# Kernel optimization log

Measured on AMD Instinct MI355X. Metric: run time of the kernel, lower is better.

The kernel has to match this reference:

```python
import jax, jax.numpy as jnp
import numpy as np

NEG_INF = -1e30  # stands in for -math.inf in masked_fill; -inf itself also works in fp32


def setup_inputs() -> dict:
    key = jax.random.key(0)
    k1, k2, k3, k4, k5 = jax.random.split(key, 5)
    B, T, S, H = 32, 512, 1024, 1024
    query = jax.random.normal(k1, (B, T, H), dtype=jnp.float32)
    encoder_outputs = jax.random.normal(k2, (S, B, H), dtype=jnp.float32)  # seq-first, as in torch RNN outputs
    src_lengths = jax.random.randint(k3, (B,), 1, S + 1, dtype=jnp.int32)
    W_in = jax.random.normal(k4, (H, H), dtype=jnp.float32) / np.sqrt(H)
    W_out = jax.random.normal(k5, (H, 2 * H), dtype=jnp.float32) / np.sqrt(2 * H)
    b_out = jnp.zeros((H,), dtype=jnp.float32)
    return {"query": query, "encoder_outputs": encoder_outputs, "src_lengths": src_lengths,
            "W_in": W_in, "W_out": W_out, "b_out": b_out}


def reference(query, encoder_outputs, src_lengths, W_in, W_out, b_out):
    # query: [B,T,H]; encoder_outputs: [S,B,H] (seq-first)
    # NOTE: the original module computes a length mask but never applies it;
    # instead it fills positions where the raw score is exactly 0 with -inf.
    z = jnp.einsum('bth,ih->bti', query, W_in)                 # linear_in (no bias)
    scores = jnp.einsum('bti,sbi->bts', z, encoder_outputs)    # bmm -> [B,T,S]
    scores = jnp.where(scores == 0, jnp.float32(-jnp.inf), scores)
    p = jax.nn.softmax(scores, axis=2)                         # [B,T,S]
    c = jnp.einsum('bts,sbh->bth', p, encoder_outputs)         # context [B,T,H]
    cat = jnp.concatenate([c, query], axis=2)                  # [B,T,2H]
    attn_h_t = jnp.tanh(jnp.einsum('btk,hk->bth', cat, W_out) + b_out)
    return attn_h_t
```

## Files before the change

### kernel.cpp

```cpp
#include <hip/hip_runtime.h>
#include <math.h>


__device__ inline unsigned short f2bf(float x) {
    unsigned int u = __float_as_uint(x);
    u += 0x7fffu + ((u >> 16) & 1u);
    return (unsigned short)(u >> 16);
}
__device__ inline float bf2f(unsigned short h) {
    return __uint_as_float(((unsigned int)h) << 16);
}
__device__ inline unsigned short f2h(float x) {
    _Float16 h = (_Float16)x;
    return *(unsigned short*)&h;
}

typedef __attribute__((ext_vector_type(8))) short    short8;
typedef __attribute__((ext_vector_type(8))) _Float16 half8;
typedef __attribute__((ext_vector_type(4))) float    f32x4;

__device__ inline void gld_lds16(const void* g, void* l) {
    __builtin_amdgcn_global_load_lds(
        (const __attribute__((address_space(1))) unsigned int*)g,
        (__attribute__((address_space(3))) unsigned int*)l, 16, 0, 0);
}

__device__ inline short8 frag_ld32(const short* Ls, int rowbase, int lane) {
    const int r = lane & 15, q = lane >> 4;
    return *(const short8*)&Ls[(rowbase + r) * 32 + ((q ^ ((r >> 1) & 3)) << 3)];
}
__device__ inline half8 frag_ld32_h(const short* Ls, int rowbase, int lane) {
    const int r = lane & 15, q = lane >> 4;
    return *(const half8*)&Ls[(rowbase + r) * 32 + ((q ^ ((r >> 1) & 3)) << 3)];
}

__device__ inline void stage_tile32(const unsigned short* g, long ld, short* lds,
                                    int rw, int lane) {
    const int lr   = lane >> 2;
    const int glog = (lane & 3) ^ ((lr >> 1) & 3);
#pragma unroll
    for (int seg = 0; seg < 2; ++seg) {
        const int row = rw + seg * 16 + lr;
        gld_lds16(g + (long)row * ld + (glog << 3), lds + (rw + seg * 16) * 32);
    }
}

__device__ inline void xcd_swz(int& bx, int& by) {
    const int gx = gridDim.x;
    const int nwg = gx * gridDim.y;
    const int lin = by * gx + bx;
    const int cpx = nwg >> 3;
    const int swz = (lin & 7) * cpx + (lin >> 3);
    bx = swz % gx;
    by = swz / gx;
}

template<int OUT_MODE, bool SWZ>
__global__ __launch_bounds__(256, 4)
void gemm_x3(const unsigned short* __restrict__ Ahg, const unsigned short* __restrict__ Alg,
             const unsigned short* __restrict__ Bhg, const unsigned short* __restrict__ Blg,
             float* __restrict__ Of, unsigned short* __restrict__ Oh,
             unsigned short* __restrict__ Ol,
             int K, long lda, long ldb, long ldc, long sA, long sB, long sC)
{
    __shared__ short Ah[128 * 32], Al[128 * 32], Bh[128 * 32], Bl[128 * 32];

    const int tid  = threadIdx.x;
    const int wave = tid >> 6, lane = tid & 63;
    const int wm = (wave & 1) << 6, wn = (wave >> 1) << 6;
    int bxi = blockIdx.x, byi = blockIdx.y;
    if constexpr (SWZ) xcd_swz(bxi, byi);
    const long m0 = (long)byi * 128, n0 = (long)bxi * 128;
    const int bz = blockIdx.z;

    const unsigned short* Ah0 = Ahg + (long)bz * sA + m0 * lda;
    const unsigned short* Al0 = Alg + (long)bz * sA + m0 * lda;
    const unsigned short* Bh0 = Bhg + (long)bz * sB + n0 * ldb;
    const unsigned short* Bl0 = Blg + (long)bz * sB + n0 * ldb;

    f32x4 acc[4][4];
#pragma unroll
    for (int i = 0; i < 4; ++i)
#pragma unroll
        for (int j = 0; j < 4; ++j) acc[i][j] = (f32x4){0.f, 0.f, 0.f, 0.f};

    const int rw = wave * 32;

    for (int k0 = 0; k0 < K; k0 += 32) {
        __syncthreads();
        stage_tile32(Ah0 + k0, lda, Ah, rw, lane);
        stage_tile32(Al0 + k0, lda, Al, rw, lane);
        stage_tile32(Bh0 + k0, ldb, Bh, rw, lane);
        stage_tile32(Bl0 + k0, ldb, Bl, rw, lane);
        __syncthreads();

        short8 ah[4], al[4], bh[4], bl[4];
#pragma unroll
        for (int i = 0; i < 4; ++i) ah[i] = frag_ld32(Ah, wm + i * 16, lane);
#pragma unroll
        for (int j = 0; j < 4; ++j) bh[j] = frag_ld32(Bh, wn + j * 16, lane);
#pragma unroll
        for (int i = 0; i < 4; ++i)
#pragma unroll
            for (int j = 0; j < 4; ++j)
                acc[i][j] = __builtin_amdgcn_mfma_f32_16x16x32_bf16(ah[i], bh[j], acc[i][j], 0, 0, 0);
#pragma unroll
        for (int j = 0; j < 4; ++j) bl[j] = frag_ld32(Bl, wn + j * 16, lane);
#pragma unroll
        for (int i = 0; i < 4; ++i)
#pragma unroll
            for (int j = 0; j < 4; ++j)
                acc[i][j] = __builtin_amdgcn_mfma_f32_16x16x32_bf16(ah[i], bl[j], acc[i][j], 0, 0, 0);
#pragma unroll
        for (int i = 0; i < 4; ++i) al[i] = frag_ld32(Al, wm + i * 16, lane);
#pragma unroll
        for (int i = 0; i < 4; ++i)
#pragma unroll
            for (int j = 0; j < 4; ++j)
                acc[i][j] = __builtin_amdgcn_mfma_f32_16x16x32_bf16(al[i], bh[j], acc[i][j], 0, 0, 0);
    }

    const int q = lane >> 4, r = lane & 15;
#pragma unroll
    for (int i = 0; i < 4; ++i)
#pragma unroll
        for (int rr = 0; rr < 4; ++rr) {
            const long grow = m0 + wm + i * 16 + q * 4 + rr;
#pragma unroll
            for (int j = 0; j < 4; ++j) {
                const long gcol = n0 + wn + j * 16 + r;
                const float v = acc[i][j][rr];
                const long off = (long)bz * sC + grow * ldc + gcol;
                if constexpr (OUT_MODE == 1) {
                    unsigned short h = f2bf(v);
                    Oh[off] = h;
                    Ol[off] = f2bf(v - bf2f(h));
                } else {
                    Of[off] = v;
                }
            }
        }
}

template<int NCHUNK, int OUT_MODE, bool SWZ>
__global__ __launch_bounds__(256, 4)
void gemm_f16(const unsigned short* __restrict__ A0, const unsigned short* __restrict__ A1,
              const unsigned short* __restrict__ B0, const unsigned short* __restrict__ B1,
              float* __restrict__ Of, unsigned short* __restrict__ Oh,
              const float* __restrict__ bias,
              int chunkK, long lda, long ldb, long ldc, long sA, long sB, long sC)
{
    __shared__ short As[128 * 32];
    __shared__ short Bs[128 * 32];

    const int tid  = threadIdx.x;
    const int wave = tid >> 6, lane = tid & 63;
    const int wm = (wave & 1) << 6, wn = (wave >> 1) << 6;
    int bxi = blockIdx.x, byi = blockIdx.y;
    if constexpr (SWZ) xcd_swz(bxi, byi);
    const long m0 = (long)byi * 128, n0 = (long)bxi * 128;
    const int bz = blockIdx.z;

    const unsigned short* Ap[2] = {A0, A1};
    const unsigned short* Bp[2] = {B0, B1};

    f32x4 acc[4][4];
#pragma unroll
    for (int i = 0; i < 4; ++i)
#pragma unroll
        for (int j = 0; j < 4; ++j) acc[i][j] = (f32x4){0.f, 0.f, 0.f, 0.f};

    const int rw = wave * 32;

#pragma unroll
    for (int c = 0; c < NCHUNK; ++c) {
        const unsigned short* Ac = Ap[c] + (long)bz * sA + m0 * lda;
        const unsigned short* Bc = Bp[c] + (long)bz * sB + n0 * ldb;
        for (int k0 = 0; k0 < chunkK; k0 += 32) {
            __syncthreads();
            stage_tile32(Ac + k0, lda, As, rw, lane);
            stage_tile32(Bc + k0, ldb, Bs, rw, lane);
            __syncthreads();

            half8 af[4], bfv[4];
#pragma unroll
            for (int i = 0; i < 4; ++i) af[i]  = frag_ld32_h(As, wm + i * 16, lane);
#pragma unroll
            for (int j = 0; j < 4; ++j) bfv[j] = frag_ld32_h(Bs, wn + j * 16, lane);
#pragma unroll
            for (int i = 0; i < 4; ++i)
#pragma unroll
                for (int j = 0; j < 4; ++j)
                    acc[i][j] = __builtin_amdgcn_mfma_f32_16x16x32_f16(af[i], bfv[j], acc[i][j], 0, 0, 0);
        }
    }

    const int q = lane >> 4, r = lane & 15;
#pragma unroll
    for (int i = 0; i < 4; ++i)
#pragma unroll
        for (int rr = 0; rr < 4; ++rr) {
            const long grow = m0 + wm + i * 16 + q * 4 + rr;
#pragma unroll
            for (int j = 0; j < 4; ++j) {
                const long gcol = n0 + wn + j * 16 + r;
                const float v = acc[i][j][rr];
                const long off = (long)bz * sC + grow * ldc + gcol;
                if constexpr (OUT_MODE == 0) {
                    Oh[off] = f2h(v);
                } else {
                    Of[off] = tanhf(v + bias[gcol]);
                }
            }
        }
}

template<bool Q16>
__global__ __launch_bounds__(256)
void split_q_k(const float* __restrict__ x, unsigned short* __restrict__ hi,
               unsigned short* __restrict__ lo, unsigned short* __restrict__ h16,
               int n4)
{
    const int i = blockIdx.x * 256 + threadIdx.x;
    if (i >= n4) return;
    const float4 v = ((const float4*)x)[i];
    ushort4 h, l;
    h.x = f2bf(v.x); h.y = f2bf(v.y); h.z = f2bf(v.z); h.w = f2bf(v.w);
    l.x = f2bf(v.x - bf2f(h.x)); l.y = f2bf(v.y - bf2f(h.y));
    l.z = f2bf(v.z - bf2f(h.z)); l.w = f2bf(v.w - bf2f(h.w));
    ((ushort4*)hi)[i] = h;
    ((ushort4*)lo)[i] = l;
    if constexpr (Q16) {
        ushort4 f;
        f.x = f2h(v.x); f.y = f2h(v.y); f.z = f2h(v.z); f.w = f2h(v.w);
        ((ushort4*)h16)[i] = f;
    }
}

__global__ __launch_bounds__(256)
void split_f32_bf16(const float* __restrict__ x, unsigned short* __restrict__ hi,
                    unsigned short* __restrict__ lo, int n4)
{
    const int i = blockIdx.x * 256 + threadIdx.x;
    if (i >= n4) return;
    const float4 v = ((const float4*)x)[i];
    ushort4 h, l;
    h.x = f2bf(v.x); h.y = f2bf(v.y); h.z = f2bf(v.z); h.w = f2bf(v.w);
    l.x = f2bf(v.x - bf2f(h.x)); l.y = f2bf(v.y - bf2f(h.y));
    l.z = f2bf(v.z - bf2f(h.z)); l.w = f2bf(v.w - bf2f(h.w));
    ((ushort4*)hi)[i] = h;
    ((ushort4*)lo)[i] = l;
}

__global__ __launch_bounds__(256)
void conv_f32_f16(const float* __restrict__ x, unsigned short* __restrict__ o, int n4)
{
    const int i = blockIdx.x * 256 + threadIdx.x;
    if (i >= n4) return;
    const float4 v = ((const float4*)x)[i];
    ushort4 h;
    h.x = f2h(v.x); h.y = f2h(v.y); h.z = f2h(v.z); h.w = f2h(v.w);
    ((ushort4*)o)[i] = h;
}

__global__ __launch_bounds__(256)
void prep_w_k(const float* __restrict__ Wi, unsigned short* __restrict__ Wih,
              unsigned short* __restrict__ Wil,
              const float* __restrict__ Wo, unsigned short* __restrict__ Wo16)
{
    const int i = blockIdx.x * 256 + threadIdx.x;
    if (i < 262144) {
        const float4 v = ((const float4*)Wi)[i];
        ushort4 h, l;
        h.x = f2bf(v.x); h.y = f2bf(v.y); h.z = f2bf(v.z); h.w = f2bf(v.w);
        l.x = f2bf(v.x - bf2f(h.x)); l.y = f2bf(v.y - bf2f(h.y));
        l.z = f2bf(v.z - bf2f(h.z)); l.w = f2bf(v.w - bf2f(h.w));
        ((ushort4*)Wih)[i] = h;
        ((ushort4*)Wil)[i] = l;
    } else {
        const int j = i - 262144;
        if (j < 524288) {
            const float4 v = ((const float4*)Wo)[j];
            ushort4 h;
            h.x = f2h(v.x); h.y = f2h(v.y); h.z = f2h(v.z); h.w = f2h(v.w);
            ((ushort4*)Wo16)[j] = h;
        }
    }
}

__global__ __launch_bounds__(256)
void split_enc_t(const float* __restrict__ E, unsigned short* __restrict__ Eh,
                 unsigned short* __restrict__ El, unsigned short* __restrict__ ET)
{
    __shared__ unsigned short L[64][72];
    const int s0 = blockIdx.x * 64, h0 = blockIdx.y * 64, b = blockIdx.z;
    const int tid = threadIdx.x;
#pragma unroll
    for (int io = 0; io < 2; ++io) {
        const int g = io * 256 + tid;
        const int rs = g >> 3, c8 = (g & 7) * 8;
        const long base = ((long)(s0 + rs) * 32 + b) * 1024 + h0 + c8;
        const float4 v0 = *(const float4*)(E + base);
        const float4 v1 = *(const float4*)(E + base + 4);
        const float vv[8] = {v0.x, v0.y, v0.z, v0.w, v1.x, v1.y, v1.z, v1.w};
        unsigned short hi[8], lo[8];
#pragma unroll
        for (int j = 0; j < 8; ++j) {
            hi[j] = f2bf(vv[j]);
            lo[j] = f2bf(vv[j] - bf2f(hi[j]));
            L[rs][c8 + j] = f2h(vv[j]);
        }
        *(ushort4*)(Eh + base)     = *(const ushort4*)&hi[0];
        *(ushort4*)(Eh + base + 4) = *(const ushort4*)&hi[4];
        *(ushort4*)(El + base)     = *(const ushort4*)&lo[0];
        *(ushort4*)(El + base + 4) = *(const ushort4*)&lo[4];
    }
    __syncthreads();
#pragma unroll
    for (int io = 0; io < 2; ++io) {
        const int g = io * 256 + tid;
        const int rh = g >> 3, c8 = (g & 7) * 8;
        unsigned short t[8];
#pragma unroll
        for (int j = 0; j < 8; ++j) t[j] = L[c8 + j][rh];
        unsigned short* dst = ET + ((long)b * 1024 + h0 + rh) * 1024 + s0 + c8;
        *(ushort4*)(dst)     = *(const ushort4*)&t[0];
        *(ushort4*)(dst + 4) = *(const ushort4*)&t[4];
    }
}

__global__ __launch_bounds__(256)
void transpose_enc_f16(const float* __restrict__ E, unsigned short* __restrict__ ET)
{
    __shared__ unsigned short L[64][72];
    const int s0 = blockIdx.x * 64, h0 = blockIdx.y * 64, b = blockIdx.z;
    const int tid = threadIdx.x;
#pragma unroll
    for (int io = 0; io < 2; ++io) {
        const int g = io * 256 + tid;
        const int rs = g >> 3, c8 = (g & 7) * 8;
        const float* src = E + ((long)(s0 + rs) * 32 + b) * 1024 + h0 + c8;
        const float4 v0 = *(const float4*)(src);
        const float4 v1 = *(const float4*)(src + 4);
        L[rs][c8 + 0] = f2h(v0.x); L[rs][c8 + 1] = f2h(v0.y);
        L[rs][c8 + 2] = f2h(v0.z); L[rs][c8 + 3] = f2h(v0.w);
        L[rs][c8 + 4] = f2h(v1.x); L[rs][c8 + 5] = f2h(v1.y);
        L[rs][c8 + 6] = f2h(v1.z); L[rs][c8 + 7] = f2h(v1.w);
    }
    __syncthreads();
#pragma unroll
    for (int io = 0; io < 2; ++io) {
        const int g = io * 256 + tid;
        const int rh = g >> 3, c8 = (g & 7) * 8;
        unsigned short t[8];
#pragma unroll
        for (int j = 0; j < 8; ++j) t[j] = L[c8 + j][rh];
        unsigned short* dst = ET + ((long)b * 1024 + h0 + rh) * 1024 + s0 + c8;
        *(ushort4*)(dst)     = *(const ushort4*)&t[0];
        *(ushort4*)(dst + 4) = *(const ushort4*)&t[4];
    }
}

__global__ __launch_bounds__(256)
void softmax_p_f16(const float* __restrict__ P, unsigned short* __restrict__ Pb)
{
    const int row  = blockIdx.x * 4 + (threadIdx.x >> 6);
    const int lane = threadIdx.x & 63;
    const float* p = P + (long)row * 1024 + lane * 4;
    unsigned short* pb = Pb + (long)row * 1024 + lane * 4;

    float4 v[4];
    float mx = -INFINITY;
#pragma unroll
    for (int i = 0; i < 4; ++i) {
        v[i] = *(const float4*)(p + i * 256);
        v[i].x = (v[i].x == 0.f) ? -INFINITY : v[i].x;
        v[i].y = (v[i].y == 0.f) ? -INFINITY : v[i].y;
        v[i].z = (v[i].z == 0.f) ? -INFINITY : v[i].z;
        v[i].w = (v[i].w == 0.f) ? -INFINITY : v[i].w;
        mx = fmaxf(mx, fmaxf(fmaxf(v[i].x, v[i].y), fmaxf(v[i].z, v[i].w)));
    }
#pragma unroll
    for (int o = 32; o > 0; o >>= 1) mx = fmaxf(mx, __shfl_xor(mx, o, 64));

    float sum = 0.f;
#pragma unroll
    for (int i = 0; i < 4; ++i) {
        v[i].x = __expf(v[i].x - mx); v[i].y = __expf(v[i].y - mx);
        v[i].z = __expf(v[i].z - mx); v[i].w = __expf(v[i].w - mx);
        sum += v[i].x + v[i].y + v[i].z + v[i].w;
    }
#pragma unroll
    for (int o = 32; o > 0; o >>= 1) sum += __shfl_xor(sum, o, 64);

    const float inv = 1.f / sum;
#pragma unroll
    for (int i = 0; i < 4; ++i) {
        ushort4 u;
        u.x = f2h(v[i].x * inv); u.y = f2h(v[i].y * inv);
        u.z = f2h(v[i].z * inv); u.w = f2h(v[i].w * inv);
        *(ushort4*)(pb + i * 256) = u;
    }
}

#define BM 128
#define BN 128
#define BKT 16

template<bool BT, bool DO_TANH, bool CAT_A>
__global__ __launch_bounds__(256)
void sgemm(const float* __restrict__ A, const float* __restrict__ A2,
           const float* __restrict__ Bmat, const float* __restrict__ bias,
           float* __restrict__ C,
           int M, int N, int K, int Ksplit,
           int lda, int ldb, int ldc,
           long sA, long sB, long sC)
{
    __shared__ float Asb[BKT][BM];
    __shared__ float Bsb[BKT][BN];

    const int bz = blockIdx.z;
    const float* Ab = A + (long)bz * sA;
    const float* Bb = Bmat + (long)bz * sB;
    float* Cb = C + (long)bz * sC;

    const int tid = threadIdx.x;
    const int m0 = blockIdx.y * BM;
    const int n0 = blockIdx.x * BN;
    const int tx = tid & 15;
    const int ty = tid >> 4;

    float acc[8][8];
#pragma unroll
    for (int i = 0; i < 8; ++i)
#pragma unroll
        for (int j = 0; j < 8; ++j) acc[i][j] = 0.f;

    for (int kk = 0; kk < K; kk += BKT) {
        const float* Asrc = Ab;
        int acol = kk;
        if constexpr (CAT_A) {
            if (kk >= Ksplit) { Asrc = A2; acol = kk - Ksplit; }
        }
#pragma unroll
        for (int i = 0; i < 2; ++i) {
            int f = i * 256 + tid;
            int row = f >> 2;
            int k4 = (f & 3) << 2;
            float4 v = *(const float4*)(Asrc + (long)(m0 + row) * lda + acol + k4);
            Asb[k4 + 0][row] = v.x; Asb[k4 + 1][row] = v.y;
            Asb[k4 + 2][row] = v.z; Asb[k4 + 3][row] = v.w;
        }
        if constexpr (BT) {
#pragma unroll
            for (int i = 0; i < 2; ++i) {
                int f = i * 256 + tid;
                int row = f >> 2;
                int k4 = (f & 3) << 2;
                float4 v = *(const float4*)(Bb + (long)(n0 + row) * ldb + kk + k4);
                Bsb[k4 + 0][row] = v.x; Bsb[k4 + 1][row] = v.y;
                Bsb[k4 + 2][row] = v.z; Bsb[k4 + 3][row] = v.w;
            }
        } else {
#pragma unroll
            for (int i = 0; i < 2; ++i) {
                int f = i * 256 + tid;
                int kr = f >> 5;
                int n4 = (f & 31) << 2;
                float4 v = *(const float4*)(Bb + (long)(kk + kr) * ldb + n0 + n4);
                *(float4*)&Bsb[kr][n4] = v;
            }
        }
        __syncthreads();
#pragma unroll
        for (int k = 0; k < BKT; ++k) {
            float a[8], bv[8];
            *(float4*)&a[0]  = *(const float4*)&Asb[k][ty * 4];
            *(float4*)&a[4]  = *(const float4*)&Asb[k][ty * 4 + 64];
            *(float4*)&bv[0] = *(const float4*)&Bsb[k][tx * 4];
            *(float4*)&bv[4] = *(const float4*)&Bsb[k][tx * 4 + 64];
#pragma unroll
            for (int i = 0; i < 8; ++i)
#pragma unroll
                for (int j = 0; j < 8; ++j)
                    acc[i][j] = fmaf(a[i], bv[j], acc[i][j]);
        }
        __syncthreads();
    }
#pragma unroll
    for (int i = 0; i < 8; ++i) {
        int rrow = m0 + ty * 4 + (i & 3) + ((i >> 2) << 6);
        float* crow = Cb + (long)rrow * ldc;
#pragma unroll
        for (int jj = 0; jj < 2; ++jj) {
            int c0 = n0 + tx * 4 + jj * 64;
            float4 v;
            v.x = acc[i][jj * 4 + 0]; v.y = acc[i][jj * 4 + 1];
            v.z = acc[i][jj * 4 + 2]; v.w = acc[i][jj * 4 + 3];
            if constexpr (DO_TANH) {
                v.x = tanhf(v.x + bias[c0 + 0]); v.y = tanhf(v.y + bias[c0 + 1]);
                v.z = tanhf(v.z + bias[c0 + 2]); v.w = tanhf(v.w + bias[c0 + 3]);
            }
            *(float4*)(crow + c0) = v;
        }
    }
}

__global__ __launch_bounds__(256)
void softmax_rows(float* __restrict__ P)
{
    const int row = blockIdx.x * 4 + (threadIdx.x >> 6);
    const int lane = threadIdx.x & 63;
    float* p = P + (long)row * 1024 + lane * 4;
    float4 v[4];
    float mx = -INFINITY;
#pragma unroll
    for (int i = 0; i < 4; ++i) {
        v[i] = *(const float4*)(p + i * 256);
        v[i].x = (v[i].x == 0.f) ? -INFINITY : v[i].x;
        v[i].y = (v[i].y == 0.f) ? -INFINITY : v[i].y;
        v[i].z = (v[i].z == 0.f) ? -INFINITY : v[i].z;
        v[i].w = (v[i].w == 0.f) ? -INFINITY : v[i].w;
        mx = fmaxf(mx, fmaxf(fmaxf(v[i].x, v[i].y), fmaxf(v[i].z, v[i].w)));
    }
#pragma unroll
    for (int o = 32; o > 0; o >>= 1) mx = fmaxf(mx, __shfl_xor(mx, o, 64));
    float sum = 0.f;
#pragma unroll
    for (int i = 0; i < 4; ++i) {
        v[i].x = __expf(v[i].x - mx); v[i].y = __expf(v[i].y - mx);
        v[i].z = __expf(v[i].z - mx); v[i].w = __expf(v[i].w - mx);
        sum += v[i].x + v[i].y + v[i].z + v[i].w;
    }
#pragma unroll
    for (int o = 32; o > 0; o >>= 1) sum += __shfl_xor(sum, o, 64);
    const float inv = 1.f / sum;
#pragma unroll
    for (int i = 0; i < 4; ++i) {
        v[i].x *= inv; v[i].y *= inv; v[i].z *= inv; v[i].w *= inv;
        *(float4*)(p + i * 256) = v[i];
    }
}

extern "C" void kernel_launch(void* const* d_in, const int* in_sizes, int n_in,
                              void* d_out, int out_size, void* d_ws, size_t ws_size,
                              hipStream_t stream)
{
    (void)in_sizes; (void)n_in; (void)out_size;
    const int Bv = 32, T = 512, S = 1024, H = 1024;

    const float* q     = (const float*)d_in[0];
    const float* enc   = (const float*)d_in[1];
    const float* W_in  = (const float*)d_in[3];
    const float* W_out = (const float*)d_in[4];
    const float* b_out = (const float*)d_in[5];
    float* out = (float*)d_out;

    const size_t need = 264ull << 20;
    if (ws_size >= need) {
        const bool big = ws_size >= (360ull << 20);

        char* w = (char*)d_ws;
        unsigned short* q_hi  = (unsigned short*)(w);
        unsigned short* q_lo  = (unsigned short*)(w + (32ull << 20));
        unsigned short* z_hi  = (unsigned short*)(w + (64ull << 20));
        unsigned short* z_lo  = (unsigned short*)(w + (96ull << 20));
        unsigned short* e_hi  = (unsigned short*)(w + (128ull << 20));
        unsigned short* e_lo  = (unsigned short*)(w + (192ull << 20));
        unsigned short* Wi_hi = (unsigned short*)(w + (256ull << 20));
        unsigned short* Wi_lo = (unsigned short*)(w + (258ull << 20));
        unsigned short* Wo16  = (unsigned short*)(w + (260ull << 20));
        unsigned short* q16b  = (unsigned short*)(w + (264ull << 20));
        unsigned short* eTb   = (unsigned short*)(w + (296ull << 20));

        unsigned short* Pb  = q_lo;
        unsigned short* q16 = big ? q16b : z_lo;
        unsigned short* eT  = big ? eTb  : e_lo;
        unsigned short* C16 = z_hi;

        if (big) split_enc_t<<<dim3(16, 16, 32), 256, 0, stream>>>(enc, e_hi, e_lo, eTb);
        else     split_f32_bf16<<<32768, 256, 0, stream>>>(enc, e_hi, e_lo, 8388608);
        prep_w_k<<<3072, 256, 0, stream>>>(W_in, Wi_hi, Wi_lo, W_out, Wo16);
        if (big) split_q_k<true ><<<16384, 256, 0, stream>>>(q, q_hi, q_lo, q16b, 4194304);
        else     split_q_k<false><<<16384, 256, 0, stream>>>(q, q_hi, q_lo, nullptr, 4194304);

        gemm_x3<1, true><<<dim3(8, 128, 1), 256, 0, stream>>>(
            q_hi, q_lo, Wi_hi, Wi_lo,
            nullptr, z_hi, z_lo,
            1024, 1024, 1024, 1024, 0, 0, 0);

        gemm_x3<2, false><<<dim3(8, 4, 32), 256, 0, stream>>>(
            z_hi, z_lo, e_hi, e_lo,
            (float*)d_out, nullptr, nullptr,
            1024, 1024, (long)Bv * H, 1024,
            (long)T * H, (long)H, (long)T * S);

        softmax_p_f16<<<(Bv * T) / 4, 256, 0, stream>>>((const float*)d_out, Pb);

        if (!big) {
            conv_f32_f16<<<16384, 256, 0, stream>>>(q, q16, 4194304);
            transpose_enc_f16<<<dim3(16, 16, 32), 256, 0, stream>>>(enc, eT);
        }

        gemm_f16<1, 0, false><<<dim3(8, 4, 32), 256, 0, stream>>>(
            Pb, nullptr, eT, nullptr,
            nullptr, C16, nullptr,
            1024, 1024, 1024, 1024,
            (long)T * S, (long)H * S, (long)T * H);

        gemm_f16<2, 3, true><<<dim3(8, 128, 1), 256, 0, stream>>>(
            C16, q16, Wo16, Wo16 + 1024,
            (float*)d_out, nullptr, b_out,
            1024, 1024, 2048, 1024, 0, 0, 0);
    } else {
        float* Z = (float*)d_ws;
        float* P = Z + (size_t)Bv * T * H;
        dim3 blk(256);
        sgemm<true, false, false><<<dim3(H / BN, (Bv * T) / BM, 1), blk, 0, stream>>>(
            q, nullptr, W_in, nullptr, Z,
            Bv * T, H, H, 0, H, H, H, 0, 0, 0);
        sgemm<true, false, false><<<dim3(S / BN, T / BM, Bv), blk, 0, stream>>>(
            Z, nullptr, enc, nullptr, P,
            T, S, H, 0, H, Bv * H, S, (long)T * H, H, (long)T * S);
        softmax_rows<<<(Bv * T) / 4, blk, 0, stream>>>(P);
        sgemm<false, false, false><<<dim3(H / BN, T / BM, Bv), blk, 0, stream>>>(
            P, nullptr, enc, nullptr, Z,
            T, H, S, 0, S, Bv * H, H, (long)T * S, H, (long)T * H);
        sgemm<true, true, true><<<dim3(H / BN, (Bv * T) / BM, 1), blk, 0, stream>>>(
            Z, q, W_out, b_out, out,
            Bv * T, H, 2 * H, H, H, 2 * H, H, 0, 0, 0);
    }
}
```

Measured before the change: 721.0 us.

## Triple-buffer GEMM K-loop with async LDS loads and 512-thread blocks

Rewrites both GEMM kernels to use 512-thread blocks with a three-stage LDS ring buffer. Global-to-LDS loads for tile t+2 are issued while tile t is computed, using explicit vmcnt waits, raw barriers and MFMA priority raising. Each wave now loads one operand tile instead of all of them and computes a 32x64 sub-tile. XCD swizzling is extended to the batched grids. This aims to hide global load latency behind MFMA work, in exchange for more LDS per block, lower occupancy and more fragile hand-written wait counts.

```diff
diff --git a/kernel.cpp b/kernel.cpp
--- a/kernel.cpp
+++ b/kernel.cpp
@@ -25,6 +25,13 @@
         (__attribute__((address_space(3))) unsigned int*)l, 16, 0, 0);
 }
 
+#define BAR() do { asm volatile("" ::: "memory"); \
+                   __builtin_amdgcn_s_barrier();  \
+                   asm volatile("" ::: "memory"); } while (0)
+#define LGKM0() do { asm volatile("s_waitcnt lgkmcnt(0)" ::: "memory"); \
+                     __builtin_amdgcn_sched_barrier(0); } while (0)
+#define VMW(n) asm volatile("s_waitcnt vmcnt(" #n ")" ::: "memory")
+
 __device__ inline short8 frag_ld32(const short* Ls, int rowbase, int lane) {
     const int r = lane & 15, q = lane >> 4;
     return *(const short8*)&Ls[(rowbase + r) * 32 + ((q ^ ((r >> 1) & 3)) << 3)];
@@ -34,8 +41,8 @@
     return *(const half8*)&Ls[(rowbase + r) * 32 + ((q ^ ((r >> 1) & 3)) << 3)];
 }
 
-__device__ inline void stage_tile32(const unsigned short* g, long ld, short* lds,
-                                    int rw, int lane) {
+__device__ inline void stage32(const unsigned short* g, long ld, short* lds,
+                               int rw, int lane) {
     const int lr   = lane >> 2;
     const int glog = (lane & 3) ^ ((lr >> 1) & 3);
 #pragma unroll
@@ -44,85 +51,121 @@
         gld_lds16(g + (long)row * ld + (glog << 3), lds + (rw + seg * 16) * 32);
     }
 }
-
-__device__ inline void xcd_swz(int& bx, int& by) {
-    const int gx = gridDim.x;
-    const int nwg = gx * gridDim.y;
-    const int lin = by * gx + bx;
-    const int cpx = nwg >> 3;
-    const int swz = (lin & 7) * cpx + (lin >> 3);
-    bx = swz % gx;
-    by = swz / gx;
-}
-
-template<int OUT_MODE, bool SWZ>
-__global__ __launch_bounds__(256, 4)
-void gemm_x3(const unsigned short* __restrict__ Ahg, const unsigned short* __restrict__ Alg,
-             const unsigned short* __restrict__ Bhg, const unsigned short* __restrict__ Blg,
-             float* __restrict__ Of, unsigned short* __restrict__ Oh,
-             unsigned short* __restrict__ Ol,
-             int K, long lda, long ldb, long ldc, long sA, long sB, long sC)
-{
-    __shared__ short Ah[128 * 32], Al[128 * 32], Bh[128 * 32], Bl[128 * 32];
+__device__ inline void stage64(const unsigned short* g, long ld, short* lds,
+                               int rw, int lane) {
+    const int lr   = lane >> 2;
+    const int glog = (lane & 3) ^ ((lr >> 1) & 3);
+#pragma unroll
+    for (int seg = 0; seg < 4; ++seg) {
+        const int row = rw + seg * 16 + lr;
+        gld_lds16(g + (long)row * ld + (glog << 3), lds + (rw + seg * 16) * 32);
+    }
+}
+
+template<int MODE>
+__device__ inline void swz3(int& bx, int& by, int& bz) {
+    if constexpr (MODE == 1) {
+        const int gx = gridDim.x;
+        const int nwg = gx * gridDim.y;
+        const int lin = by * gx + bx;
+        const int cpx = nwg >> 3;
+        const int s = (lin & 7) * cpx + (lin >> 3);
+        bx = s % gx; by = s / gx;
+    } else if constexpr (MODE == 2) {
+        const int gx = gridDim.x, gy = gridDim.y;
+        const int nwg = gx * gy * gridDim.z;
+        const int lin = (bz * gy + by) * gx + bx;
+        const int cpx = nwg >> 3;
+        const int s = (lin & 7) * cpx + (lin >> 3);
+        bx = s % gx; by = (s / gx) % gy; bz = s / (gx * gy);
+    }
+}
+
+template<int OUT_MODE, int SWZ>
+__global__ __launch_bounds__(512, 2)
+void gemm_x3p(const unsigned short* __restrict__ Ahg, const unsigned short* __restrict__ Alg,
+              const unsigned short* __restrict__ Bhg, const unsigned short* __restrict__ Blg,
+              float* __restrict__ Of, unsigned short* __restrict__ Oh,
+              unsigned short* __restrict__ Ol,
+              int NT, long lda, long ldb, long ldc, long sA, long sB, long sC)
+{
+    __shared__ short SL[3 * 4 * 4096];
 
     const int tid  = threadIdx.x;
     const int wave = tid >> 6, lane = tid & 63;
-    const int wm = (wave & 1) << 6, wn = (wave >> 1) << 6;
-    int bxi = blockIdx.x, byi = blockIdx.y;
-    if constexpr (SWZ) xcd_swz(bxi, byi);
+    const int wm = (wave & 3) << 5;
+    const int wn = (wave >> 2) << 6;
+    int bxi = blockIdx.x, byi = blockIdx.y, bzi = blockIdx.z;
+    swz3<SWZ>(bxi, byi, bzi);
     const long m0 = (long)byi * 128, n0 = (long)bxi * 128;
-    const int bz = blockIdx.z;
-
-    const unsigned short* Ah0 = Ahg + (long)bz * sA + m0 * lda;
-    const unsigned short* Al0 = Alg + (long)bz * sA + m0 * lda;
-    const unsigned short* Bh0 = Bhg + (long)bz * sB + n0 * ldb;
-    const unsigned short* Bl0 = Blg + (long)bz * sB + n0 * ldb;
-
-    f32x4 acc[4][4];
-#pragma unroll
-    for (int i = 0; i < 4; ++i)
+
+    const int wtile = wave >> 1;
+    const int wrow  = (wave & 1) << 6;
+    const unsigned short* gA = (wtile == 0) ? Ahg : Alg;
+    const unsigned short* gB = (wtile == 2) ? Bhg : Blg;
+    const unsigned short* g0 = (wtile < 2)
+        ? gA + (long)bzi * sA + m0 * lda
+        : gB + (long)bzi * sB + n0 * ldb;
+    const long gld = (wtile < 2) ? lda : ldb;
+
+    f32x4 acc[2][4];
+#pragma unroll
+    for (int i = 0; i < 2; ++i)
 #pragma unroll
         for (int j = 0; j < 4; ++j) acc[i][j] = (f32x4){0.f, 0.f, 0.f, 0.f};
 
-    const int rw = wave * 32;
-
-    for (int k0 = 0; k0 < K; k0 += 32) {
-        __syncthreads();
-        stage_tile32(Ah0 + k0, lda, Ah, rw, lane);
-        stage_tile32(Al0 + k0, lda, Al, rw, lane);
-        stage_tile32(Bh0 + k0, ldb, Bh, rw, lane);
-        stage_tile32(Bl0 + k0, ldb, Bl, rw, lane);
-        __syncthreads();
-
-        short8 ah[4], al[4], bh[4], bl[4];
-#pragma unroll
-        for (int i = 0; i < 4; ++i) ah[i] = frag_ld32(Ah, wm + i * 16, lane);
-#pragma unroll
-        for (int j = 0; j < 4; ++j) bh[j] = frag_ld32(Bh, wn + j * 16, lane);
-#pragma unroll
-        for (int i = 0; i < 4; ++i)
+    stage64(g0,      gld, SL + 0 * 16384 + wtile * 4096, wrow, lane);
+    stage64(g0 + 32, gld, SL + 1 * 16384 + wtile * 4096, wrow, lane);
+    VMW(4);
+    BAR();
+
+    for (int t = 0; t < NT; ++t) {
+        const int s = t % 3;
+        const short* As = SL + s * 16384;
+
+        const bool st = (t + 2) < NT;
+        if (st) {
+            const int s2 = (t + 2) % 3;
+            stage64(g0 + (long)(t + 2) * 32, gld,
+                    SL + s2 * 16384 + wtile * 4096, wrow, lane);
+        }
+
+        short8 ah[2], al[2], bh[4], bl[4];
+#pragma unroll
+        for (int i = 0; i < 2; ++i) ah[i] = frag_ld32(As + 0 * 4096, wm + i * 16, lane);
+#pragma unroll
+        for (int i = 0; i < 2; ++i) al[i] = frag_ld32(As + 1 * 4096, wm + i * 16, lane);
+#pragma unroll
+        for (int j = 0; j < 4; ++j) bh[j] = frag_ld32(As + 2 * 4096, wn + j * 16, lane);
+#pragma unroll
+        for (int j = 0; j < 4; ++j) bl[j] = frag_ld32(As + 3 * 4096, wn + j * 16, lane);
+
+        if (st) { VMW(4); } else { VMW(0); }
+        BAR();
+        LGKM0();
+        __builtin_amdgcn_s_setprio(1);
+#pragma unroll
+        for (int i = 0; i < 2; ++i)
 #pragma unroll
             for (int j = 0; j < 4; ++j)
                 acc[i][j] = __builtin_amdgcn_mfma_f32_16x16x32_bf16(ah[i], bh[j], acc[i][j], 0, 0, 0);
 #pragma unroll
-        for (int j = 0; j < 4; ++j) bl[j] = frag_ld32(Bl, wn + j * 16, lane);
-#pragma unroll
-        for (int i = 0; i < 4; ++i)
+        for (int i = 0; i < 2; ++i)
 #pragma unroll
             for (int j = 0; j < 4; ++j)
                 acc[i][j] = __builtin_amdgcn_mfma_f32_16x16x32_bf16(ah[i], bl[j], acc[i][j], 0, 0, 0);
 #pragma unroll
-        for (int i = 0; i < 4; ++i) al[i] = frag_ld32(Al, wm + i * 16, lane);
-#pragma unroll
-        for (int i = 0; i < 4; ++i)
+        for (int i = 0; i < 2; ++i)
 #pragma unroll
             for (int j = 0; j < 4; ++j)
                 acc[i][j] = __builtin_amdgcn_mfma_f32_16x16x32_bf16(al[i], bh[j], acc[i][j], 0, 0, 0);
+        __builtin_amdgcn_s_setprio(0);
+        BAR();
     }
 
     const int q = lane >> 4, r = lane & 15;
 #pragma unroll
-    for (int i = 0; i < 4; ++i)
+    for (int i = 0; i < 2; ++i)
 #pragma unroll
         for (int rr = 0; rr < 4; ++rr) {
             const long grow = m0 + wm + i * 16 + q * 4 + rr;
@@ -130,7 +173,7 @@
             for (int j = 0; j < 4; ++j) {
                 const long gcol = n0 + wn + j * 16 + r;
                 const float v = acc[i][j][rr];
-                const long off = (long)bz * sC + grow * ldc + gcol;
+                const long off = (long)bzi * sC + grow * ldc + gcol;
                 if constexpr (OUT_MODE == 1) {
                     unsigned short h = f2bf(v);
                     Oh[off] = h;
@@ -142,62 +185,79 @@
         }
 }
 
-template<int NCHUNK, int OUT_MODE, bool SWZ>
-__global__ __launch_bounds__(256, 4)
-void gemm_f16(const unsigned short* __restrict__ A0, const unsigned short* __restrict__ A1,
-              const unsigned short* __restrict__ B0, const unsigned short* __restrict__ B1,
-              float* __restrict__ Of, unsigned short* __restrict__ Oh,
-              const float* __restrict__ bias,
-              int chunkK, long lda, long ldb, long ldc, long sA, long sB, long sC)
-{
-    __shared__ short As[128 * 32];
-    __shared__ short Bs[128 * 32];
+template<int NCHUNK, int OUT_MODE, int SWZ>
+__global__ __launch_bounds__(512, 2)
+void gemm_f16p(const unsigned short* __restrict__ A0, const unsigned short* __restrict__ A1,
+               const unsigned short* __restrict__ B0, const unsigned short* __restrict__ B1,
+               float* __restrict__ Of, unsigned short* __restrict__ Oh,
+               const float* __restrict__ bias,
+               int NT, long lda, long ldb, long ldc, long sA, long sB, long sC)
+{
+    __shared__ short SL[3 * 2 * 4096];
 
     const int tid  = threadIdx.x;
     const int wave = tid >> 6, lane = tid & 63;
-    const int wm = (wave & 1) << 6, wn = (wave >> 1) << 6;
-    int bxi = blockIdx.x, byi = blockIdx.y;
-    if constexpr (SWZ) xcd_swz(bxi, byi);
+    const int wm = (wave & 3) << 5;
+    const int wn = (wave >> 2) << 6;
+    int bxi = blockIdx.x, byi = blockIdx.y, bzi = blockIdx.z;
+    swz3<SWZ>(bxi, byi, bzi);
     const long m0 = (long)byi * 128, n0 = (long)bxi * 128;
-    const int bz = blockIdx.z;
-
-    const unsigned short* Ap[2] = {A0, A1};
-    const unsigned short* Bp[2] = {B0, B1};
-
-    f32x4 acc[4][4];
-#pragma unroll
-    for (int i = 0; i < 4; ++i)
+
+    const int wtile = wave >> 2;
+    const int wrow  = (wave & 3) << 5;
+    const long gld  = (wtile == 0) ? lda : ldb;
+    const long gbase = (wtile == 0) ? ((long)bzi * sA + m0 * lda)
+                                    : ((long)bzi * sB + n0 * ldb);
+    const unsigned short* gc0 = ((wtile == 0) ? A0 : B0) + gbase;
+    const unsigned short* gc1 = ((NCHUNK > 1) ? ((wtile == 0) ? A1 : B1) : nullptr);
+    if (NCHUNK > 1 && gc1) gc1 += gbase;
+
+    f32x4 acc[2][4];
+#pragma unroll
+    for (int i = 0; i < 2; ++i)
 #pragma unroll
         for (int j = 0; j < 4; ++j) acc[i][j] = (f32x4){0.f, 0.f, 0.f, 0.f};
 
-    const int rw = wave * 32;
-
-#pragma unroll
-    for (int c = 0; c < NCHUNK; ++c) {
-        const unsigned short* Ac = Ap[c] + (long)bz * sA + m0 * lda;
-        const unsigned short* Bc = Bp[c] + (long)bz * sB + n0 * ldb;
-        for (int k0 = 0; k0 < chunkK; k0 += 32) {
-            __syncthreads();
-            stage_tile32(Ac + k0, lda, As, rw, lane);
-            stage_tile32(Bc + k0, ldb, Bs, rw, lane);
-            __syncthreads();
-
-            half8 af[4], bfv[4];
-#pragma unroll
-            for (int i = 0; i < 4; ++i) af[i]  = frag_ld32_h(As, wm + i * 16, lane);
-#pragma unroll
-            for (int j = 0; j < 4; ++j) bfv[j] = frag_ld32_h(Bs, wn + j * 16, lane);
-#pragma unroll
-            for (int i = 0; i < 4; ++i)
-#pragma unroll
-                for (int j = 0; j < 4; ++j)
-                    acc[i][j] = __builtin_amdgcn_mfma_f32_16x16x32_f16(af[i], bfv[j], acc[i][j], 0, 0, 0);
-        }
+    stage32(gc0,      gld, SL + 0 * 8192 + wtile * 4096, wrow, lane);
+    stage32(gc0 + 32, gld, SL + 1 * 8192 + wtile * 4096, wrow, lane);
+    VMW(2);
+    BAR();
+
+    for (int t = 0; t < NT; ++t) {
+        const int s = t % 3;
+        const short* As = SL + s * 8192;
+
+        const bool st = (t + 2) < NT;
+        if (st) {
+            const int t2 = t + 2;
+            const unsigned short* gc = (NCHUNK > 1 && t2 >= 32) ? gc1 : gc0;
+            const long kk = (long)(t2 & 31) << 5;
+            const int s2 = t2 % 3;
+            stage32(gc + kk, gld, SL + s2 * 8192 + wtile * 4096, wrow, lane);
+        }
+
+        half8 af[2], bf[4];
+#pragma unroll
+        for (int i = 0; i < 2; ++i) af[i] = frag_ld32_h(As + 0 * 4096, wm + i * 16, lane);
+#pragma unroll
+        for (int j = 0; j < 4; ++j) bf[j] = frag_ld32_h(As + 1 * 4096, wn + j * 16, lane);
+
+        if (st) { VMW(2); } else { VMW(0); }
+        BAR();
+        LGKM0();
+        __builtin_amdgcn_s_setprio(1);
+#pragma unroll
+        for (int i = 0; i < 2; ++i)
+#pragma unroll
+            for (int j = 0; j < 4; ++j)
+                acc[i][j] = __builtin_amdgcn_mfma_f32_16x16x32_f16(af[i], bf[j], acc[i][j], 0, 0, 0);
+        __builtin_amdgcn_s_setprio(0);
+        BAR();
     }
 
     const int q = lane >> 4, r = lane & 15;
 #pragma unroll
-    for (int i = 0; i < 4; ++i)
+    for (int i = 0; i < 2; ++i)
 #pragma unroll
         for (int rr = 0; rr < 4; ++rr) {
             const long grow = m0 + wm + i * 16 + q * 4 + rr;
@@ -205,7 +265,7 @@
             for (int j = 0; j < 4; ++j) {
                 const long gcol = n0 + wn + j * 16 + r;
                 const float v = acc[i][j][rr];
-                const long off = (long)bz * sC + grow * ldc + gcol;
+                const long off = (long)bzi * sC + grow * ldc + gcol;
                 if constexpr (OUT_MODE == 0) {
                     Oh[off] = f2h(v);
                 } else {
@@ -584,15 +644,15 @@
         if (big) split_q_k<true ><<<16384, 256, 0, stream>>>(q, q_hi, q_lo, q16b, 4194304);
         else     split_q_k<false><<<16384, 256, 0, stream>>>(q, q_hi, q_lo, nullptr, 4194304);
 
-        gemm_x3<1, true><<<dim3(8, 128, 1), 256, 0, stream>>>(
+        gemm_x3p<1, 1><<<dim3(8, 128, 1), 512, 0, stream>>>(
             q_hi, q_lo, Wi_hi, Wi_lo,
             nullptr, z_hi, z_lo,
-            1024, 1024, 1024, 1024, 0, 0, 0);
-
-        gemm_x3<2, false><<<dim3(8, 4, 32), 256, 0, stream>>>(
+            32, 1024, 1024, 1024, 0, 0, 0);
+
+        gemm_x3p<2, 2><<<dim3(8, 4, 32), 512, 0, stream>>>(
             z_hi, z_lo, e_hi, e_lo,
             (float*)d_out, nullptr, nullptr,
-            1024, 1024, (long)Bv * H, 1024,
+            32, 1024, (long)Bv * H, 1024,
             (long)T * H, (long)H, (long)T * S);
 
         softmax_p_f16<<<(Bv * T) / 4, 256, 0, stream>>>((const float*)d_out, Pb);
@@ -602,16 +662,16 @@
             transpose_enc_f16<<<dim3(16, 16, 32), 256, 0, stream>>>(enc, eT);
         }
 
-        gemm_f16<1, 0, false><<<dim3(8, 4, 32), 256, 0, stream>>>(
+        gemm_f16p<1, 0, 2><<<dim3(8, 4, 32), 512, 0, stream>>>(
             Pb, nullptr, eT, nullptr,
             nullptr, C16, nullptr,
-            1024, 1024, 1024, 1024,
+            32, 1024, 1024, 1024,
             (long)T * S, (long)H * S, (long)T * H);
 
-        gemm_f16<2, 3, true><<<dim3(8, 128, 1), 256, 0, stream>>>(
+        gemm_f16p<2, 3, 1><<<dim3(8, 128, 1), 512, 0, stream>>>(
             C16, q16, Wo16, Wo16 + 1024,
             (float*)d_out, nullptr, b_out,
-            1024, 1024, 2048, 1024, 0, 0, 0);
+            64, 1024, 2048, 1024, 0, 0, 0);
     } else {
         float* Z = (float*)d_ws;
         float* P = Z + (size_t)Bv * T * H;
```

Result: slower. 753.1 us (+4.5%).
